# Kernel optimization log

Hardware: AMD Instinct MI355X
Metric: run time of the kernel (lower is better)

Reference implementation:

```python
import jax, jax.numpy as jnp
import numpy as np

B, C, H, W_ = 128, 2048, 14, 14
N_DESC, N_ANS = 32, 1845


def setup_inputs() -> dict:
    key = jax.random.key(0)
    k1, k2, k3, k4, k5 = jax.random.split(key, 5)
    mask = jax.random.uniform(k1, (B, 1, H, W_), dtype=jnp.float32)
    features = jax.random.normal(k2, (B, C, H, W_), dtype=jnp.float32)
    instance = jax.random.randint(k3, (B,), 0, N_DESC, dtype=jnp.int64)
    Wt = jax.random.normal(k4, (N_DESC, N_ANS, C), dtype=jnp.float32) * 0.02
    b = jax.random.normal(k5, (N_DESC, N_ANS), dtype=jnp.float32) * 0.02
    return {"mask": mask, "features": features, "instance": instance, "W": Wt, "b": b}


def reference(mask, features, instance, W, b):
    Bsz, Cc, Hh, Ww = features.shape
    feat_flat = features.reshape(Bsz, Cc, Hh * Ww)            # [B,C,HW]
    mask_flat = mask.reshape(Bsz, 1, Hh * Ww)                 # [B,1,HW]
    attended = jnp.mean(mask_flat * feat_flat, axis=2)        # [B,C]
    Wi = W[instance]                                          # [B,A,C] per-sample weight gather
    bi = b[instance]                                          # [B,A]
    preds = jnp.einsum('bc,bac->ba', attended, Wi) + bi       # grouped small GEMM
    return preds
```

## Files before the change

kernel.cpp:

```cpp
#include <hip/hip_runtime.h>

#define BSZ   128
#define CC    2048
#define HW    196
#define NDESC 32
#define NANS  1845

__global__ void group_kernel(const int* __restrict__ inst,
                             int* __restrict__ counts,
                             int* __restrict__ lists) {
    int t = threadIdx.x;
    if (t < NDESC) counts[t] = 0;
    __syncthreads();
    int i = inst[t];
    int slot = atomicAdd(&counts[i], 1);
    lists[i * BSZ + slot] = t;
}

__global__ __launch_bounds__(256) void attend_kernel(
        const float* __restrict__ mask,
        const float* __restrict__ feat,
        float* __restrict__ attended) {
    int row  = blockIdx.x * 4 + (threadIdx.x >> 6);
    int lane = threadIdx.x & 63;
    int b    = row >> 11;

    const float* frow = feat + (size_t)row * HW;
    const float* mrow = mask + (size_t)b * HW;

    float partial = 0.f;
    if (lane < 49) {
        float4 f = *(const float4*)(frow + lane * 4);
        float4 m = *(const float4*)(mrow + lane * 4);
        partial = f.x * m.x + f.y * m.y + f.z * m.z + f.w * m.w;
    }
    #pragma unroll
    for (int off = 32; off; off >>= 1)
        partial += __shfl_xor(partial, off, 64);

    if (lane == 0) attended[row] = partial * (1.f / 196.f);
}

#define ATILES ((NANS + 7) / 8)

__global__ __launch_bounds__(256) void gemm_kernel(
        const float* __restrict__ attended,
        const float* __restrict__ W,
        const float* __restrict__ bias,
        const int* __restrict__ counts,
        const int* __restrict__ lists,
        float* __restrict__ out) {
    int inst = blockIdx.x / ATILES;
    int tile = blockIdx.x % ATILES;
    int cnt  = counts[inst];
    if (cnt == 0) return;

    int wid  = threadIdx.x >> 6;
    int lane = threadIdx.x & 63;
    int a0   = tile * 8 + wid * 2;
    int a1   = a0 + 1;
    bool v0  = a0 < NANS;
    bool v1  = a1 < NANS;

    const float* Wb = W + (size_t)inst * NANS * CC;

    float4 w0[8], w1[8];
    if (v0) {
        const float* wr = Wb + (size_t)a0 * CC + lane * 4;
        #pragma unroll
        for (int k = 0; k < 8; ++k) w0[k] = *(const float4*)(wr + k * 256);
    }
    if (v1) {
        const float* wr = Wb + (size_t)a1 * CC + lane * 4;
        #pragma unroll
        for (int k = 0; k < 8; ++k) w1[k] = *(const float4*)(wr + k * 256);
    }
    float b0 = v0 ? bias[inst * NANS + a0] : 0.f;
    float b1 = v1 ? bias[inst * NANS + a1] : 0.f;

    for (int j = 0; j < cnt; ++j) {
        int bj = lists[inst * BSZ + j];
        const float* ar = attended + (size_t)bj * CC + lane * 4;
        float acc0 = 0.f, acc1 = 0.f;
        #pragma unroll
        for (int k = 0; k < 8; ++k) {
            float4 a4 = *(const float4*)(ar + k * 256);
            if (v0) acc0 += a4.x * w0[k].x + a4.y * w0[k].y
                          + a4.z * w0[k].z + a4.w * w0[k].w;
            if (v1) acc1 += a4.x * w1[k].x + a4.y * w1[k].y
                          + a4.z * w1[k].z + a4.w * w1[k].w;
        }
        #pragma unroll
        for (int off = 32; off; off >>= 1) {
            acc0 += __shfl_xor(acc0, off, 64);
            acc1 += __shfl_xor(acc1, off, 64);
        }
        if (lane == 0) {
            if (v0) out[(size_t)bj * NANS + a0] = acc0 + b0;
            if (v1) out[(size_t)bj * NANS + a1] = acc1 + b1;
        }
    }
}

extern "C" void kernel_launch(void* const* d_in, const int* in_sizes, int n_in,
                              void* d_out, int out_size, void* d_ws, size_t ws_size,
                              hipStream_t stream) {
    const float* mask = (const float*)d_in[0];
    const float* feat = (const float*)d_in[1];
    const int*   inst = (const int*)d_in[2];
    const float* W    = (const float*)d_in[3];
    const float* bias = (const float*)d_in[4];
    float*       out  = (float*)d_out;

    float* attended = (float*)d_ws;
    int*   counts   = (int*)((char*)d_ws + (size_t)BSZ * CC * sizeof(float));
    int*   lists    = counts + NDESC;

    group_kernel<<<1, BSZ, 0, stream>>>(inst, counts, lists);
    attend_kernel<<<(BSZ * CC) / 4, 256, 0, stream>>>(mask, feat, attended);
    gemm_kernel<<<NDESC * ATILES, 256, 0, stream>>>(attended, W, bias,
                                                    counts, lists, out);
}
```

Baseline: 729.6 us.

## Fuse grouping into attend kernel, stream W nontemporally, process two samples per iteration

Removes the separate single-block grouping launch by running the instance bucketing in block 0 of the attention kernel. W rows are now loaded with nontemporal hints so the streamed weights do not evict the reused attended vectors. The GEMM loop handles two samples per iteration, giving more independent loads and FMAs in flight. This adds register pressure and a tail predicate for odd counts.

```diff
diff --git a/kernel.cpp b/kernel.cpp
--- a/kernel.cpp
+++ b/kernel.cpp
@@ -5,43 +5,46 @@
 #define HW    196
 #define NDESC 32
 #define NANS  1845
+#define ATILES ((NANS + 7) / 8)
 
-__global__ void group_kernel(const int* __restrict__ inst,
-                             int* __restrict__ counts,
-                             int* __restrict__ lists) {
-    int t = threadIdx.x;
-    if (t < NDESC) counts[t] = 0;
-    __syncthreads();
-    int i = inst[t];
-    int slot = atomicAdd(&counts[i], 1);
-    lists[i * BSZ + slot] = t;
-}
+typedef float f4 __attribute__((ext_vector_type(4)));
 
-__global__ __launch_bounds__(256) void attend_kernel(
+__global__ __launch_bounds__(256) void attend_group_kernel(
         const float* __restrict__ mask,
         const float* __restrict__ feat,
-        float* __restrict__ attended) {
+        const int*  __restrict__ inst,
+        float* __restrict__ attended,
+        int* __restrict__ counts,
+        int* __restrict__ lists) {
     int row  = blockIdx.x * 4 + (threadIdx.x >> 6);
     int lane = threadIdx.x & 63;
     int b    = row >> 11;
 
-    const float* frow = feat + (size_t)row * HW;
-    const float* mrow = mask + (size_t)b * HW;
+    const f4* frow = (const f4*)(feat + (size_t)row * HW);
+    const f4* mrow = (const f4*)(mask + (size_t)b * HW);
 
     float partial = 0.f;
     if (lane < 49) {
-        float4 f = *(const float4*)(frow + lane * 4);
-        float4 m = *(const float4*)(mrow + lane * 4);
+        f4 f = frow[lane];
+        f4 m = mrow[lane];
         partial = f.x * m.x + f.y * m.y + f.z * m.z + f.w * m.w;
     }
     #pragma unroll
     for (int off = 32; off; off >>= 1)
         partial += __shfl_xor(partial, off, 64);
+    if (lane == 0) attended[row] = partial * (1.f / 196.f);
 
-    if (lane == 0) attended[row] = partial * (1.f / 196.f);
+    if (blockIdx.x == 0) {
+        int t = threadIdx.x;
+        if (t < NDESC) counts[t] = 0;
+        __syncthreads();
+        if (t < BSZ) {
+            int i = inst[t];
+            int slot = atomicAdd(&counts[i], 1);
+            lists[i * BSZ + slot] = t;
+        }
+    }
 }
-
-#define ATILES ((NANS + 7) / 8)
 
 __global__ __launch_bounds__(256) void gemm_kernel(
         const float* __restrict__ attended,
@@ -50,9 +53,9 @@
         const int* __restrict__ counts,
         const int* __restrict__ lists,
         float* __restrict__ out) {
-    int inst = blockIdx.x / ATILES;
+    int ins  = blockIdx.x / ATILES;
     int tile = blockIdx.x % ATILES;
-    int cnt  = counts[inst];
+    int cnt  = counts[ins];
     if (cnt == 0) return;
 
     int wid  = threadIdx.x >> 6;
@@ -62,42 +65,55 @@
     bool v0  = a0 < NANS;
     bool v1  = a1 < NANS;
 
-    const float* Wb = W + (size_t)inst * NANS * CC;
+    const float* Wb = W + (size_t)ins * NANS * CC;
 
-    float4 w0[8], w1[8];
+    f4 w0[8], w1[8];
     if (v0) {
-        const float* wr = Wb + (size_t)a0 * CC + lane * 4;
+        const f4* wr = (const f4*)(Wb + (size_t)a0 * CC) + lane;
         #pragma unroll
-        for (int k = 0; k < 8; ++k) w0[k] = *(const float4*)(wr + k * 256);
+        for (int k = 0; k < 8; ++k) w0[k] = __builtin_nontemporal_load(wr + k * 64);
     }
     if (v1) {
-        const float* wr = Wb + (size_t)a1 * CC + lane * 4;
+        const f4* wr = (const f4*)(Wb + (size_t)a1 * CC) + lane;
         #pragma unroll
-        for (int k = 0; k < 8; ++k) w1[k] = *(const float4*)(wr + k * 256);
+        for (int k = 0; k < 8; ++k) w1[k] = __builtin_nontemporal_load(wr + k * 64);
     }
-    float b0 = v0 ? bias[inst * NANS + a0] : 0.f;
-    float b1 = v1 ? bias[inst * NANS + a1] : 0.f;
+    float b0 = v0 ? bias[ins * NANS + a0] : 0.f;
+    float b1 = v1 ? bias[ins * NANS + a1] : 0.f;
 
-    for (int j = 0; j < cnt; ++j) {
-        int bj = lists[inst * BSZ + j];
-        const float* ar = attended + (size_t)bj * CC + lane * 4;
-        float acc0 = 0.f, acc1 = 0.f;
+    const int* lst = lists + ins * BSZ;
+
+    for (int j = 0; j < cnt; j += 2) {
+        int  bj0 = lst[j];
+        bool h1  = (j + 1) < cnt;
+        int  bj1 = h1 ? lst[j + 1] : bj0;
+        const f4* ar0 = (const f4*)(attended + (size_t)bj0 * CC) + lane;
+        const f4* ar1 = (const f4*)(attended + (size_t)bj1 * CC) + lane;
+
+        float acc00 = 0.f, acc01 = 0.f, acc10 = 0.f, acc11 = 0.f;
         #pragma unroll
         for (int k = 0; k < 8; ++k) {
-            float4 a4 = *(const float4*)(ar + k * 256);
-            if (v0) acc0 += a4.x * w0[k].x + a4.y * w0[k].y
-                          + a4.z * w0[k].z + a4.w * w0[k].w;
-            if (v1) acc1 += a4.x * w1[k].x + a4.y * w1[k].y
-                          + a4.z * w1[k].z + a4.w * w1[k].w;
+            f4 x = ar0[k * 64];
+            f4 y = ar1[k * 64];
+            acc00 += x.x * w0[k].x + x.y * w0[k].y + x.z * w0[k].z + x.w * w0[k].w;
+            acc01 += x.x * w1[k].x + x.y * w1[k].y + x.z * w1[k].z + x.w * w1[k].w;
+            acc10 += y.x * w0[k].x + y.y * w0[k].y + y.z * w0[k].z + y.w * w0[k].w;
+            acc11 += y.x * w1[k].x + y.y * w1[k].y + y.z * w1[k].z + y.w * w1[k].w;
         }
         #pragma unroll
         for (int off = 32; off; off >>= 1) {
-            acc0 += __shfl_xor(acc0, off, 64);
-            acc1 += __shfl_xor(acc1, off, 64);
+            acc00 += __shfl_xor(acc00, off, 64);
+            acc01 += __shfl_xor(acc01, off, 64);
+            acc10 += __shfl_xor(acc10, off, 64);
+            acc11 += __shfl_xor(acc11, off, 64);
         }
         if (lane == 0) {
-            if (v0) out[(size_t)bj * NANS + a0] = acc0 + b0;
-            if (v1) out[(size_t)bj * NANS + a1] = acc1 + b1;
+            if (v0) out[(size_t)bj0 * NANS + a0] = acc00 + b0;
+            if (v1) out[(size_t)bj0 * NANS + a1] = acc01 + b1;
+            if (h1) {
+                if (v0) out[(size_t)bj1 * NANS + a0] = acc10 + b0;
+                if (v1) out[(size_t)bj1 * NANS + a1] = acc11 + b1;
+            }
         }
     }
 }
@@ -116,8 +132,8 @@
     int*   counts   = (int*)((char*)d_ws + (size_t)BSZ * CC * sizeof(float));
     int*   lists    = counts + NDESC;
 
-    group_kernel<<<1, BSZ, 0, stream>>>(inst, counts, lists);
-    attend_kernel<<<(BSZ * CC) / 4, 256, 0, stream>>>(mask, feat, attended);
-    gemm_kernel<<<NDESC * ATILES, 256, 0, stream>>>(attended, W, bias,
-                                                    counts, lists, out);
+    attend_group_kernel<<<(BSZ * CC) / 4, 256, 0, stream>>>(
+        mask, feat, inst, attended, counts, lists);
+    gemm_kernel<<<NDESC * ATILES, 256, 0, stream>>>(
+        attended, W, bias, counts, lists, out);
 }
```

New measurement: 745.1 us. 2.1% more time.
